# Optimization experiments

Measured on AMD Instinct MI355X. Metric: run time of the kernel, lower is better.

The kernel has to match this reference:

```python
import jax, jax.numpy as jnp
import numpy as np

IDIM = 128
C = 3
NB_SAMPLES = 128
R = 32768
SH_C0 = 0.28209479177387814
SH_C1 = 0.4886025119029199
SH_C2 = np.array([1.0925484305920792, -1.0925484305920792, 0.31539156525252005,
                  -1.0925484305920792, 0.5462742152960396], dtype=np.float32)


def eval_sh_bases(d):
    # d: (R,3) unit directions -> (R,9) degree-2 real SH basis
    x, y, z = d[:, 0], d[:, 1], d[:, 2]
    return jnp.stack([
        jnp.full_like(x, SH_C0),
        -SH_C1 * y, SH_C1 * z, -SH_C1 * x,
        SH_C2[0] * x * y, SH_C2[1] * y * z,
        SH_C2[2] * (2.0 * z * z - x * x - y * y),
        SH_C2[3] * x * z, SH_C2[4] * (x * x - y * y)], axis=-1)


def trilerp(pts, grid):
    # pts: (N,3) in voxel coords (box_min=0, delta_voxel=1); grid: (D,D,D,F)
    D = grid.shape[0]
    p = jnp.clip(pts, 0.0, D - 1 - 1e-4)
    i0 = jnp.floor(p).astype(jnp.int32)
    w = p - i0.astype(p.dtype)          # (N,3) fractional weights
    i1 = jnp.minimum(i0 + 1, D - 1)
    out = jnp.zeros((pts.shape[0], grid.shape[-1]), dtype=p.dtype)
    for dx in (0, 1):
        wx = w[:, 0] if dx else 1.0 - w[:, 0]
        ix = i1[:, 0] if dx else i0[:, 0]
        for dy in (0, 1):
            wy = w[:, 1] if dy else 1.0 - w[:, 1]
            iy = i1[:, 1] if dy else i0[:, 1]
            for dz in (0, 1):
                wz = w[:, 2] if dz else 1.0 - w[:, 2]
                iz = i1[:, 2] if dz else i0[:, 2]
                out = out + (wx * wy * wz)[:, None] * grid[ix, iy, iz]
    return out


def setup_inputs() -> dict:
    key = jax.random.key(0)
    k = jax.random.split(key, 6)
    x = jax.random.uniform(k[0], (R, 3), jnp.float32) * (IDIM - 1)
    d = jax.random.normal(k[1], (R, 3), jnp.float32)
    d = d / jnp.linalg.norm(d, axis=1, keepdims=True)
    tmin = jax.random.uniform(k[2], (R,), jnp.float32) * 5.0
    tmax = tmin + 20.0 + jax.random.uniform(k[3], (R,), jnp.float32) * 80.0
    grid = jax.random.uniform(k[4], (IDIM, IDIM, IDIM, 9 * C), jnp.float32)
    opacity = jax.random.uniform(k[5], (IDIM, IDIM, IDIM, 1), jnp.float32)
    return {"x": x, "d": d, "tmin": tmin, "tmax": tmax, "grid": grid, "opacity": opacity}


def reference(x, d, tmin, tmax, grid, opacity):
    nb_rays = x.shape[0]
    # samples = arange(0.05, 0.95, 1/nb_samples): S entries
    S = int(np.floor(0.9 * NB_SAMPLES - 1e-6)) + 1
    base = 0.05 + jnp.arange(S, dtype=x.dtype) / NB_SAMPLES            # (S,)
    samples = (tmax - tmin)[:, None] * base[None, :] + tmin[:, None]   # (R,S)
    pts = x[:, None, :] + samples[..., None] * d[:, None, :]           # (R,S,3)
    sh = eval_sh_bases(d)                                              # (R,9)
    flat = pts.reshape(-1, 3)
    coeffs = trilerp(flat, grid).reshape(nb_rays, S, C, 9)             # (R,S,C,9)
    op = jnp.clip(trilerp(flat, opacity), 0.0, 100000.0).reshape(nb_rays, S)
    harm = coeffs * sh[:, None, None, :]                               # (R,S,C,9)
    samples_color = jnp.clip(harm.sum(axis=3) + 0.5, 0.0, 100000.0)    # (R,S,C)
    deltas = samples[:, 1:] - samples[:, :-1]                          # (R,S-1)
    dts = -(deltas * op[:, :-1])
    cum = jnp.concatenate([jnp.zeros((nb_rays, 1), dtype=x.dtype),
                           jnp.cumsum(dts, axis=1)[:, :-1]], axis=1)
    w = jnp.exp(cum) * (1.0 - jnp.exp(dts))                            # (R,S-1)
    rays_color = jnp.sum(w[..., None] * samples_color[:, :-1, :], axis=1)  # (R,C)
    return rays_color
```

## Files before the change

kernel.cpp:

```cpp
#include <hip/hip_runtime.h>

#define NS 115
#define WEPS 5e-5f
#define LOG_TSKIP -6.9078f
#define NCELLS (128*128*128)
#define PACK_BYTES ((size_t)NCELLS * 64)
#define PACK_THREADS (2048 * 256)
#define PACK_ITERS ((NCELLS * 4) / PACK_THREADS)

typedef float f32x4 __attribute__((ext_vector_type(4)));
typedef float f32x2 __attribute__((ext_vector_type(2)));
typedef _Float16 h16x8 __attribute__((ext_vector_type(8)));
typedef _Float16 h16x4 __attribute__((ext_vector_type(4)));

struct SH9 { float a,b,c,d,e,f,g,h,i; };

__device__ __forceinline__ f32x4 load4(const float* p) { f32x4 v; __builtin_memcpy(&v, p, 16); return v; }
__device__ __forceinline__ f32x2 load2(const float* p) { f32x2 v; __builtin_memcpy(&v, p, 8);  return v; }
__device__ __forceinline__ h16x8 load8h(const _Float16* p) { h16x8 v; __builtin_memcpy(&v, p, 16); return v; }
__device__ __forceinline__ h16x4 load4h(const _Float16* p) { h16x4 v; __builtin_memcpy(&v, p, 8);  return v; }
__device__ __forceinline__ f32x4 ntload4(const float* p) {
    return __builtin_nontemporal_load((const f32x4*)p);
}

__device__ __forceinline__ void pos_to_cell(float px, float py, float pz,
                                            int& ibase, float* wxs, float* wys, float* wzs) {
    px = fminf(fmaxf(px, 0.0f), 126.9999f);
    py = fminf(fmaxf(py, 0.0f), 126.9999f);
    pz = fminf(fmaxf(pz, 0.0f), 126.9999f);
    int ix = (int)px, iy = (int)py, iz = (int)pz;
    float wx = px - (float)ix, wy = py - (float)iy, wz = pz - (float)iz;
    ibase = (ix << 14) + (iy << 7) + iz;
    wxs[0] = 1.0f - wx; wxs[1] = wx;
    wys[0] = 1.0f - wy; wys[1] = wy;
    wzs[0] = 1.0f - wz; wzs[1] = wz;
}

__device__ __forceinline__ float eval_op(float px, float py, float pz,
                                         const float* __restrict__ opa) {
    int ibase; float wxs[2], wys[2], wzs[2];
    pos_to_cell(px, py, pz, ibase, wxs, wys, wzs);
    float op = 0.0f;
    #pragma unroll
    for (int cx = 0; cx < 2; ++cx)
    #pragma unroll
    for (int cy = 0; cy < 2; ++cy) {
        int idx = ibase + (cx << 14) + (cy << 7);
        f32x2 pr = load2(opa + idx);
        float wxy = wxs[cx] * wys[cy];
        op = fmaf(wxy * wzs[0], pr.x, op);
        op = fmaf(wxy * wzs[1], pr.y, op);
    }
    return fminf(fmaxf(op, 0.0f), 100000.0f);
}

__device__ __forceinline__ void eval_color_h(float px, float py, float pz,
                                             const _Float16* __restrict__ pack,
                                             const SH9& sh,
                                             float& cr, float& cg, float& cb) {
    int ibase; float wxs[2], wys[2], wzs[2];
    pos_to_cell(px, py, pz, ibase, wxs, wys, wzs);
    float r = 0.0f, g = 0.0f, b = 0.0f;
    #pragma unroll
    for (int cx = 0; cx < 2; ++cx)
    #pragma unroll
    for (int cy = 0; cy < 2; ++cy)
    #pragma unroll
    for (int cz = 0; cz < 2; ++cz) {
        int idx = ibase + (cx << 14) + (cy << 7) + cz;
        float wc = wxs[cx] * wys[cy] * wzs[cz];
        const _Float16* cp = pack + ((size_t)idx << 5);
        h16x8 v0 = load8h(cp);
        h16x8 v1 = load8h(cp + 8);
        h16x8 v2 = load8h(cp + 16);
        h16x4 v3 = load4h(cp + 24);
        float c0 = sh.a*(float)v0[0] + sh.b*(float)v0[1] + sh.c*(float)v0[2] + sh.d*(float)v0[3]
                 + sh.e*(float)v0[4] + sh.f*(float)v0[5] + sh.g*(float)v0[6] + sh.h*(float)v0[7]
                 + sh.i*(float)v1[0];
        float c1 = sh.a*(float)v1[1] + sh.b*(float)v1[2] + sh.c*(float)v1[3] + sh.d*(float)v1[4]
                 + sh.e*(float)v1[5] + sh.f*(float)v1[6] + sh.g*(float)v1[7] + sh.h*(float)v2[0]
                 + sh.i*(float)v2[1];
        float c2 = sh.a*(float)v2[2] + sh.b*(float)v2[3] + sh.c*(float)v2[4] + sh.d*(float)v2[5]
                 + sh.e*(float)v2[6] + sh.f*(float)v2[7] + sh.g*(float)v3[0] + sh.h*(float)v3[1]
                 + sh.i*(float)v3[2];
        r = fmaf(wc, c0, r);
        g = fmaf(wc, c1, g);
        b = fmaf(wc, c2, b);
    }
    cr = fminf(fmaxf(r + 0.5f, 0.0f), 100000.0f);
    cg = fminf(fmaxf(g + 0.5f, 0.0f), 100000.0f);
    cb = fminf(fmaxf(b + 0.5f, 0.0f), 100000.0f);
}

__device__ __forceinline__ void eval_color_f(float px, float py, float pz,
                                             const float* __restrict__ grid,
                                             const SH9& sh,
                                             float& cr, float& cg, float& cb) {
    int ibase; float wxs[2], wys[2], wzs[2];
    pos_to_cell(px, py, pz, ibase, wxs, wys, wzs);
    float r = 0.0f, g = 0.0f, b = 0.0f;
    #pragma unroll
    for (int cx = 0; cx < 2; ++cx)
    #pragma unroll
    for (int cy = 0; cy < 2; ++cy)
    #pragma unroll
    for (int cz = 0; cz < 2; ++cz) {
        int idx = ibase + (cx << 14) + (cy << 7) + cz;
        float wc = wxs[cx] * wys[cy] * wzs[cz];
        const float* cp = grid + (size_t)idx * 27;
        f32x4 v0 = load4(cp);
        f32x4 v1 = load4(cp + 4);
        f32x4 v2 = load4(cp + 8);
        f32x4 v3 = load4(cp + 12);
        f32x4 v4 = load4(cp + 16);
        f32x4 v5 = load4(cp + 20);
        f32x4 v6 = load4(cp + 23);
        float c0 = sh.a*v0.x + sh.b*v0.y + sh.c*v0.z + sh.d*v0.w
                 + sh.e*v1.x + sh.f*v1.y + sh.g*v1.z + sh.h*v1.w + sh.i*v2.x;
        float c1 = sh.a*v2.y + sh.b*v2.z + sh.c*v2.w + sh.d*v3.x
                 + sh.e*v3.y + sh.f*v3.z + sh.g*v3.w + sh.h*v4.x + sh.i*v4.y;
        float c2 = sh.a*v4.z + sh.b*v4.w + sh.c*v5.x + sh.d*v5.y
                 + sh.e*v5.z + sh.f*v5.w + sh.g*v6.y + sh.h*v6.z + sh.i*v6.w;
        r = fmaf(wc, c0, r);
        g = fmaf(wc, c1, g);
        b = fmaf(wc, c2, b);
    }
    cr = fminf(fmaxf(r + 0.5f, 0.0f), 100000.0f);
    cg = fminf(fmaxf(g + 0.5f, 0.0f), 100000.0f);
    cb = fminf(fmaxf(b + 0.5f, 0.0f), 100000.0f);
}

__device__ __forceinline__ float wave_incl_scan(float v, int lane) {
    #pragma unroll
    for (int off = 1; off < 64; off <<= 1) {
        float n = __shfl_up(v, (unsigned)off, 64);
        if (lane >= off) v += n;
    }
    return v;
}

__device__ __forceinline__ void pack_one(const float* __restrict__ grid,
                                         _Float16* __restrict__ pack, int o) {
    int cell = o >> 2;
    int q = o & 3;
    int base = cell * 27;
    int offa = base + ((q == 3) ? 23 : q * 8);
    int offb = (q == 3) ? offa : offa + 4;
    f32x4 a = ntload4(grid + offa);
    f32x4 b = ntload4(grid + offb);
    h16x8 out;
    if (q == 3) {
        out[0] = (_Float16)a.y; out[1] = (_Float16)a.z; out[2] = (_Float16)a.w;
        out[3] = (_Float16)0.f; out[4] = (_Float16)0.f; out[5] = (_Float16)0.f;
        out[6] = (_Float16)0.f; out[7] = (_Float16)0.f;
    } else {
        out[0] = (_Float16)a.x; out[1] = (_Float16)a.y; out[2] = (_Float16)a.z; out[3] = (_Float16)a.w;
        out[4] = (_Float16)b.x; out[5] = (_Float16)b.y; out[6] = (_Float16)b.z; out[7] = (_Float16)b.w;
    }
    __builtin_memcpy(pack + ((size_t)o << 3), &out, 16);
}

__global__ __launch_bounds__(256) void pack_kernel(const float* __restrict__ grid,
                                                   _Float16* __restrict__ pack) {
    int tid = blockIdx.x * blockDim.x + threadIdx.x;
    #pragma unroll 1
    for (int i = 0; i < PACK_ITERS; i += 4) {
        #pragma unroll
        for (int j = 0; j < 4; ++j) {
            pack_one(grid, pack, tid + (i + j) * PACK_THREADS);
        }
    }
}

template <bool PACKED>
__global__ __launch_bounds__(256) void rf_kernel(
    const float* __restrict__ x, const float* __restrict__ d,
    const float* __restrict__ tmin, const float* __restrict__ tmax,
    const float* __restrict__ grid, const _Float16* __restrict__ pack,
    const float* __restrict__ opa,
    float* __restrict__ out, int nrays)
{
    int gtid = blockIdx.x * blockDim.x + threadIdx.x;
    int ray = __builtin_amdgcn_readfirstlane(gtid >> 6);
    int lane = threadIdx.x & 63;
    if (ray >= nrays) return;

    float ox = x[3*ray+0], oy = x[3*ray+1], oz = x[3*ray+2];
    float ddx = d[3*ray+0], ddy = d[3*ray+1], ddz = d[3*ray+2];
    float t0 = tmin[ray], t1 = tmax[ray];
    float range = t1 - t0;
    float delta = range * 0.0078125f;

    SH9 sh;
    sh.a = 0.28209479177387814f;
    sh.b = -0.4886025119029199f * ddy;
    sh.c =  0.4886025119029199f * ddz;
    sh.d = -0.4886025119029199f * ddx;
    sh.e =  1.0925484305920792f * ddx * ddy;
    sh.f = -1.0925484305920792f * ddy * ddz;
    sh.g =  0.31539156525252005f * (2.0f*ddz*ddz - ddx*ddx - ddy*ddy);
    sh.h = -1.0925484305920792f * ddx * ddz;
    sh.i =  0.5462742152960396f * (ddx*ddx - ddy*ddy);

    float accR = 0.0f, accG = 0.0f, accB = 0.0f;

    {
        int s = lane;
        float t = range * (0.05f + (float)s * 0.0078125f) + t0;
        float px = ox + t*ddx, py = oy + t*ddy, pz = oz + t*ddz;
        float opv = eval_op(px, py, pz, opa);
        float dts = -delta * opv;
        float incl = wave_incl_scan(dts, lane);
        float cum = incl - dts;
        float total0 = __shfl(incl, 63, 64);
        float w = __expf(cum) * (1.0f - __expf(dts));
        if (w > WEPS) {
            float cr, cg, cb;
            if (PACKED) eval_color_h(px, py, pz, pack, sh, cr, cg, cb);
            else        eval_color_f(px, py, pz, grid, sh, cr, cg, cb);
            accR = w * cr; accG = w * cg; accB = w * cb;
        }
        if (total0 > LOG_TSKIP) {
            int s1 = 64 + lane;
            float dts1 = 0.0f;
            float px1 = 0.f, py1 = 0.f, pz1 = 0.f;
            if (s1 < NS) {
                float t1s = range * (0.05f + (float)s1 * 0.0078125f) + t0;
                px1 = ox + t1s*ddx; py1 = oy + t1s*ddy; pz1 = oz + t1s*ddz;
                float opv1 = eval_op(px1, py1, pz1, opa);
                dts1 = -delta * opv1;
            }
            float incl1 = wave_incl_scan(dts1, lane);
            float cum1 = total0 + incl1 - dts1;
            float w1 = __expf(cum1) * (1.0f - __expf(dts1));
            if (w1 > WEPS) {
                float cr, cg, cb;
                if (PACKED) eval_color_h(px1, py1, pz1, pack, sh, cr, cg, cb);
                else        eval_color_f(px1, py1, pz1, grid, sh, cr, cg, cb);
                accR = fmaf(w1, cr, accR);
                accG = fmaf(w1, cg, accG);
                accB = fmaf(w1, cb, accB);
            }
        }
    }

    #pragma unroll
    for (int off = 32; off > 0; off >>= 1) {
        accR += __shfl_xor(accR, off, 64);
        accG += __shfl_xor(accG, off, 64);
        accB += __shfl_xor(accB, off, 64);
    }
    if (lane == 0) {
        out[3*ray+0] = accR;
        out[3*ray+1] = accG;
        out[3*ray+2] = accB;
    }
}

extern "C" void kernel_launch(void* const* d_in, const int* in_sizes, int n_in,
                              void* d_out, int out_size, void* d_ws, size_t ws_size,
                              hipStream_t stream) {
    const float* x    = (const float*)d_in[0];
    const float* d    = (const float*)d_in[1];
    const float* tmin = (const float*)d_in[2];
    const float* tmax = (const float*)d_in[3];
    const float* grid = (const float*)d_in[4];
    const float* opa  = (const float*)d_in[5];
    float* out = (float*)d_out;

    int nrays = in_sizes[0] / 3;
    int threads = 256;
    int blocks = (nrays * 64 + threads - 1) / threads;

    if (ws_size >= PACK_BYTES) {
        _Float16* pack = (_Float16*)d_ws;
        pack_kernel<<<PACK_THREADS / 256, 256, 0, stream>>>(grid, pack);
        rf_kernel<true><<<blocks, threads, 0, stream>>>(x, d, tmin, tmax, grid, pack, opa, out, nrays);
    } else {
        rf_kernel<false><<<blocks, threads, 0, stream>>>(x, d, tmin, tmax, grid, nullptr, opa, out, nrays);
    }
}
```

Measured before the change: 408.1 us.

## Fuse opacity/weight pass into pack kernel and split color into separate kernel

Moves the opacity trilerp, transmittance scan and per-sample weight computation into the grid-packing kernel, where each wave handles four rays after finishing its pack work. The weights are written to a workspace buffer, and a second kernel reads them and does only the packed fp16 color lookups. The aim is to overlap the latency-bound opacity pass with the bandwidth-bound packing and to shorten the color kernel. In exchange it adds an extra global write and read of 128 weights per ray, and the pack kernel's opacity work runs at low occupancy with only 2048 blocks.

New measurement: 400.0 us. 2.0% less time.

```diff
diff --git a/kernel.cpp b/kernel.cpp
--- a/kernel.cpp
+++ b/kernel.cpp
@@ -5,7 +5,11 @@
 #define LOG_TSKIP -6.9078f
 #define NCELLS (128*128*128)
 #define PACK_BYTES ((size_t)NCELLS * 64)
-#define PACK_THREADS (2048 * 256)
+#define NRAYS_C 32768
+#define WBUF_BYTES ((size_t)NRAYS_C * 128 * 4)
+#define NEED_BYTES (PACK_BYTES + WBUF_BYTES)
+#define PACK_BLOCKS 2048
+#define PACK_THREADS (PACK_BLOCKS * 256)
 #define PACK_ITERS ((NCELLS * 4) / PACK_THREADS)
 
 typedef float f32x4 __attribute__((ext_vector_type(4)));
@@ -139,6 +143,20 @@
     return v;
 }
 
+__device__ __forceinline__ SH9 make_sh(float ddx, float ddy, float ddz) {
+    SH9 sh;
+    sh.a = 0.28209479177387814f;
+    sh.b = -0.4886025119029199f * ddy;
+    sh.c =  0.4886025119029199f * ddz;
+    sh.d = -0.4886025119029199f * ddx;
+    sh.e =  1.0925484305920792f * ddx * ddy;
+    sh.f = -1.0925484305920792f * ddy * ddz;
+    sh.g =  0.31539156525252005f * (2.0f*ddz*ddz - ddx*ddx - ddy*ddy);
+    sh.h = -1.0925484305920792f * ddx * ddz;
+    sh.i =  0.5462742152960396f * (ddx*ddx - ddy*ddy);
+    return sh;
+}
+
 __device__ __forceinline__ void pack_one(const float* __restrict__ grid,
                                          _Float16* __restrict__ pack, int o) {
     int cell = o >> 2;
@@ -160,24 +178,65 @@
     __builtin_memcpy(pack + ((size_t)o << 3), &out, 16);
 }
 
-__global__ __launch_bounds__(256) void pack_kernel(const float* __restrict__ grid,
-                                                   _Float16* __restrict__ pack) {
-    int tid = blockIdx.x * blockDim.x + threadIdx.x;
-    #pragma unroll 1
-    for (int i = 0; i < PACK_ITERS; i += 4) {
-        #pragma unroll
-        for (int j = 0; j < 4; ++j) {
-            pack_one(grid, pack, tid + (i + j) * PACK_THREADS);
-        }
-    }
-}
-
-template <bool PACKED>
-__global__ __launch_bounds__(256) void rf_kernel(
+__global__ __launch_bounds__(256) void pack_op_kernel(
+    const float* __restrict__ grid, _Float16* __restrict__ pack,
     const float* __restrict__ x, const float* __restrict__ d,
     const float* __restrict__ tmin, const float* __restrict__ tmax,
-    const float* __restrict__ grid, const _Float16* __restrict__ pack,
-    const float* __restrict__ opa,
+    const float* __restrict__ opa, float* __restrict__ wbuf, int nrays)
+{
+    const int t = threadIdx.x;
+    const int tid = blockIdx.x * 256 + t;
+
+    #pragma unroll 1
+    for (int i = 0; i < PACK_ITERS; i += 8) {
+        #pragma unroll
+        for (int j = 0; j < 8; ++j)
+            pack_one(grid, pack, tid + (i + j) * PACK_THREADS);
+    }
+
+    const int wave = tid >> 6;
+    const int lane = t & 63;
+    #pragma unroll 1
+    for (int r = 0; r < 4; ++r) {
+        int ray = __builtin_amdgcn_readfirstlane(wave * 4 + r);
+        if (ray >= nrays) break;
+        float ox = x[3*ray+0], oy = x[3*ray+1], oz = x[3*ray+2];
+        float ddx = d[3*ray+0], ddy = d[3*ray+1], ddz = d[3*ray+2];
+        float t0 = tmin[ray], t1 = tmax[ray];
+        float range = t1 - t0;
+        float delta = range * 0.0078125f;
+
+        float tt = range * (0.05f + (float)lane * 0.0078125f) + t0;
+        float px = ox + tt*ddx, py = oy + tt*ddy, pz = oz + tt*ddz;
+        float opv = eval_op(px, py, pz, opa);
+        float dts = -delta * opv;
+        float incl = wave_incl_scan(dts, lane);
+        float cum = incl - dts;
+        float total0 = __shfl(incl, 63, 64);
+        float w = __expf(cum) * (1.0f - __expf(dts));
+        wbuf[ray * 128 + lane] = w;
+
+        float w1 = 0.0f;
+        if (total0 > LOG_TSKIP) {
+            int s1 = 64 + lane;
+            float dts1 = 0.0f;
+            if (s1 < NS) {
+                float t1s = range * (0.05f + (float)s1 * 0.0078125f) + t0;
+                float qx = ox + t1s*ddx, qy = oy + t1s*ddy, qz = oz + t1s*ddz;
+                dts1 = -delta * eval_op(qx, qy, qz, opa);
+            }
+            float incl1 = wave_incl_scan(dts1, lane);
+            float cum1 = total0 + incl1 - dts1;
+            w1 = __expf(cum1) * (1.0f - __expf(dts1));
+        }
+        wbuf[ray * 128 + 64 + lane] = w1;
+    }
+}
+
+__global__ __launch_bounds__(256) void color_kernel(
+    const float* __restrict__ x, const float* __restrict__ d,
+    const float* __restrict__ tmin, const float* __restrict__ tmax,
+    const _Float16* __restrict__ pack, const float* __restrict__ wbuf,
     float* __restrict__ out, int nrays)
 {
     int gtid = blockIdx.x * blockDim.x + threadIdx.x;
@@ -189,25 +248,64 @@
     float ddx = d[3*ray+0], ddy = d[3*ray+1], ddz = d[3*ray+2];
     float t0 = tmin[ray], t1 = tmax[ray];
     float range = t1 - t0;
+    SH9 sh = make_sh(ddx, ddy, ddz);
+
+    float w0 = wbuf[ray * 128 + lane];
+    float w1 = wbuf[ray * 128 + 64 + lane];
+
+    float accR = 0.0f, accG = 0.0f, accB = 0.0f;
+    if (w0 > WEPS) {
+        float tt = range * (0.05f + (float)lane * 0.0078125f) + t0;
+        float px = ox + tt*ddx, py = oy + tt*ddy, pz = oz + tt*ddz;
+        float cr, cg, cb;
+        eval_color_h(px, py, pz, pack, sh, cr, cg, cb);
+        accR = w0 * cr; accG = w0 * cg; accB = w0 * cb;
+    }
+    if (w1 > WEPS) {
+        float t1s = range * (0.05f + (float)(64 + lane) * 0.0078125f) + t0;
+        float px = ox + t1s*ddx, py = oy + t1s*ddy, pz = oz + t1s*ddz;
+        float cr, cg, cb;
+        eval_color_h(px, py, pz, pack, sh, cr, cg, cb);
+        accR = fmaf(w1, cr, accR);
+        accG = fmaf(w1, cg, accG);
+        accB = fmaf(w1, cb, accB);
+    }
+
+    #pragma unroll
+    for (int off = 32; off > 0; off >>= 1) {
+        accR += __shfl_xor(accR, off, 64);
+        accG += __shfl_xor(accG, off, 64);
+        accB += __shfl_xor(accB, off, 64);
+    }
+    if (lane == 0) {
+        out[3*ray+0] = accR;
+        out[3*ray+1] = accG;
+        out[3*ray+2] = accB;
+    }
+}
+
+__global__ __launch_bounds__(256) void rf_fallback(
+    const float* __restrict__ x, const float* __restrict__ d,
+    const float* __restrict__ tmin, const float* __restrict__ tmax,
+    const float* __restrict__ grid, const float* __restrict__ opa,
+    float* __restrict__ out, int nrays)
+{
+    int gtid = blockIdx.x * blockDim.x + threadIdx.x;
+    int ray = __builtin_amdgcn_readfirstlane(gtid >> 6);
+    int lane = threadIdx.x & 63;
+    if (ray >= nrays) return;
+
+    float ox = x[3*ray+0], oy = x[3*ray+1], oz = x[3*ray+2];
+    float ddx = d[3*ray+0], ddy = d[3*ray+1], ddz = d[3*ray+2];
+    float t0 = tmin[ray], t1 = tmax[ray];
+    float range = t1 - t0;
     float delta = range * 0.0078125f;
-
-    SH9 sh;
-    sh.a = 0.28209479177387814f;
-    sh.b = -0.4886025119029199f * ddy;
-    sh.c =  0.4886025119029199f * ddz;
-    sh.d = -0.4886025119029199f * ddx;
-    sh.e =  1.0925484305920792f * ddx * ddy;
-    sh.f = -1.0925484305920792f * ddy * ddz;
-    sh.g =  0.31539156525252005f * (2.0f*ddz*ddz - ddx*ddx - ddy*ddy);
-    sh.h = -1.0925484305920792f * ddx * ddz;
-    sh.i =  0.5462742152960396f * (ddx*ddx - ddy*ddy);
+    SH9 sh = make_sh(ddx, ddy, ddz);
 
     float accR = 0.0f, accG = 0.0f, accB = 0.0f;
-
     {
-        int s = lane;
-        float t = range * (0.05f + (float)s * 0.0078125f) + t0;
-        float px = ox + t*ddx, py = oy + t*ddy, pz = oz + t*ddz;
+        float tt = range * (0.05f + (float)lane * 0.0078125f) + t0;
+        float px = ox + tt*ddx, py = oy + tt*ddy, pz = oz + tt*ddz;
         float opv = eval_op(px, py, pz, opa);
         float dts = -delta * opv;
         float incl = wave_incl_scan(dts, lane);
@@ -216,8 +314,7 @@
         float w = __expf(cum) * (1.0f - __expf(dts));
         if (w > WEPS) {
             float cr, cg, cb;
-            if (PACKED) eval_color_h(px, py, pz, pack, sh, cr, cg, cb);
-            else        eval_color_f(px, py, pz, grid, sh, cr, cg, cb);
+            eval_color_f(px, py, pz, grid, sh, cr, cg, cb);
             accR = w * cr; accG = w * cg; accB = w * cb;
         }
         if (total0 > LOG_TSKIP) {
@@ -227,23 +324,20 @@
             if (s1 < NS) {
                 float t1s = range * (0.05f + (float)s1 * 0.0078125f) + t0;
                 px1 = ox + t1s*ddx; py1 = oy + t1s*ddy; pz1 = oz + t1s*ddz;
-                float opv1 = eval_op(px1, py1, pz1, opa);
-                dts1 = -delta * opv1;
+                dts1 = -delta * eval_op(px1, py1, pz1, opa);
             }
             float incl1 = wave_incl_scan(dts1, lane);
             float cum1 = total0 + incl1 - dts1;
             float w1 = __expf(cum1) * (1.0f - __expf(dts1));
             if (w1 > WEPS) {
                 float cr, cg, cb;
-                if (PACKED) eval_color_h(px1, py1, pz1, pack, sh, cr, cg, cb);
-                else        eval_color_f(px1, py1, pz1, grid, sh, cr, cg, cb);
+                eval_color_f(px1, py1, pz1, grid, sh, cr, cg, cb);
                 accR = fmaf(w1, cr, accR);
                 accG = fmaf(w1, cg, accG);
                 accB = fmaf(w1, cb, accB);
             }
         }
     }
-
     #pragma unroll
     for (int off = 32; off > 0; off >>= 1) {
         accR += __shfl_xor(accR, off, 64);
@@ -269,14 +363,14 @@
     float* out = (float*)d_out;
 
     int nrays = in_sizes[0] / 3;
-    int threads = 256;
-    int blocks = (nrays * 64 + threads - 1) / threads;
-
-    if (ws_size >= PACK_BYTES) {
+    int blocks = (nrays * 64 + 255) / 256;
+
+    if (ws_size >= NEED_BYTES && nrays <= NRAYS_C) {
         _Float16* pack = (_Float16*)d_ws;
-        pack_kernel<<<PACK_THREADS / 256, 256, 0, stream>>>(grid, pack);
-        rf_kernel<true><<<blocks, threads, 0, stream>>>(x, d, tmin, tmax, grid, pack, opa, out, nrays);
+        float* wbuf = (float*)((char*)d_ws + PACK_BYTES);
+        pack_op_kernel<<<PACK_BLOCKS, 256, 0, stream>>>(grid, pack, x, d, tmin, tmax, opa, wbuf, nrays);
+        color_kernel<<<blocks, 256, 0, stream>>>(x, d, tmin, tmax, pack, wbuf, out, nrays);
     } else {
-        rf_kernel<false><<<blocks, threads, 0, stream>>>(x, d, tmin, tmax, grid, nullptr, opa, out, nrays);
-    }
-}
+        rf_fallback<<<blocks, 256, 0, stream>>>(x, d, tmin, tmax, grid, opa, out, nrays);
+    }
+}
```
